# Kernel tuning notes

Measured on AMD Instinct MI355X. Metric: run time of the kernel, lower is better.

## Reference

```python
import jax, jax.numpy as jnp
import numpy as np

N = 8192  # input_size
DT = 1.0
TAU1, TAU2, TAU3 = 20.0, 50.0, 100.0


def _corr(a, b):
    # Pearson correlation of two equal-length vectors (torch.corrcoef[0,1]), NaN -> 0
    ac = a - jnp.mean(a)
    bc = b - jnp.mean(b)
    c = jnp.sum(ac * bc) / jnp.sqrt(jnp.sum(ac * ac) * jnp.sum(bc * bc))
    return jnp.where(jnp.isnan(c), jnp.zeros_like(c), c)


def setup_inputs() -> dict:
    key = jax.random.key(0)
    ks = jax.random.split(key, 8)
    return {
        'sensory_motor_input': jax.random.normal(ks[0], (N,), jnp.float32),
        'layer1_state': jax.random.normal(ks[1], (N,), jnp.float32),
        'layer2_state': jax.random.normal(ks[2], (N // 2,), jnp.float32),
        'layer3_state': jax.random.normal(ks[3], (N // 4,), jnp.float32),
        'w12': jax.random.normal(ks[4], (N // 2, N), jnp.float32) * 0.1,
        'w23': jax.random.normal(ks[5], (N // 4, N // 2), jnp.float32) * 0.1,
        'w32': jax.random.normal(ks[6], (N // 2, N // 4), jnp.float32) * 0.1,
        'w21': jax.random.normal(ks[7], (N, N // 2), jnp.float32) * 0.1,
        'correlation_strength': jnp.zeros((), jnp.float32),
        'neural_coherence': jnp.zeros((), jnp.float32),
    }


def reference(sensory_motor_input, layer1_state, layer2_state, layer3_state,
              w12, w23, w32, w21, correlation_strength, neural_coherence):
    # Layer 1: direct sensorimotor, exponential decay toward tanh target
    l1_target = jnp.tanh(sensory_motor_input)
    d1 = 1.0 - DT / TAU1
    l1 = d1 * layer1_state + (1.0 - d1) * l1_target

    # Layer 2: bottom-up + 0.3 * top-down feedback
    l2_in = w12 @ l1 + 0.3 * (w32 @ layer3_state)
    d2 = 1.0 - DT / TAU2
    l2 = d2 * layer2_state + (1.0 - d2) * jnp.tanh(l2_in)

    # Layer 3: meta feedback
    d3 = 1.0 - DT / TAU3
    l3 = d3 * layer3_state + (1.0 - d3) * jnp.tanh(w23 @ l2)

    # Cross-layer correlations (truncate the larger vector)
    c12 = _corr(l1[: l2.shape[0]], l2)
    c23 = _corr(l2[: l3.shape[0]], l3)
    corr_new = 0.9 * correlation_strength + 0.1 * (c12 + c23) / 2.0

    total_activity = jnp.sum(jnp.abs(l1)) + jnp.sum(jnp.abs(l2)) + jnp.sum(jnp.abs(l3))
    activity_variance = jnp.var(jnp.concatenate([l1, l2, l3]), ddof=1)  # torch.var unbiased
    coherence = total_activity / (activity_variance + 1e-6)
    coh_new = 0.9 * neural_coherence + 0.1 * jnp.clip(coherence, 0.0, 10.0)

    hier_activity = total_activity / (N + N // 2 + N // 4)
    return (l1, l2, l3, corr_new, coh_new, hier_activity)
```

## Files before the change

### kernel.cpp

```cpp
#include <hip/hip_runtime.h>
#include <math.h>

#define N1 8192
#define N2 4096
#define N3 2048

typedef float f4 __attribute__((ext_vector_type(4)));

__global__ __launch_bounds__(256) void k_l1(const float* __restrict__ smi,
                                            const float* __restrict__ l1s,
                                            float* __restrict__ l1) {
    int i = blockIdx.x * 256 + threadIdx.x;
    if (i < N1) l1[i] = 0.95f * l1s[i] + 0.05f * tanhf(smi[i]);
}

__global__ __launch_bounds__(256) void k_l2(const float* __restrict__ w12,
                                            const float* __restrict__ w32,
                                            const float* __restrict__ l1,
                                            const float* __restrict__ l3s,
                                            const float* __restrict__ l2s,
                                            float* __restrict__ l2) {
    __shared__ float ws[4][2];
    const int r0 = blockIdx.x * 2;
    const int t = threadIdx.x;
    const f4* __restrict__ w12r0 = reinterpret_cast<const f4*>(w12) + (size_t)r0 * (N1 / 4);
    const f4* __restrict__ w12r1 = w12r0 + (N1 / 4);
    const f4* __restrict__ w32r0 = reinterpret_cast<const f4*>(w32) + (size_t)r0 * (N3 / 4);
    const f4* __restrict__ w32r1 = w32r0 + (N3 / 4);
    const f4* __restrict__ x1 = reinterpret_cast<const f4*>(l1);
    const f4* __restrict__ x3 = reinterpret_cast<const f4*>(l3s);

    float a0 = 0.0f, a1 = 0.0f, b0 = 0.0f, b1 = 0.0f;
#pragma unroll
    for (int k = 0; k < (N1 / 4) / 256; ++k) {
        const int i = t + k * 256;
        f4 x = x1[i];
        f4 u = __builtin_nontemporal_load(&w12r0[i]);
        f4 v = __builtin_nontemporal_load(&w12r1[i]);
        a0 = fmaf(u.x, x.x, fmaf(u.y, x.y, fmaf(u.z, x.z, fmaf(u.w, x.w, a0))));
        a1 = fmaf(v.x, x.x, fmaf(v.y, x.y, fmaf(v.z, x.z, fmaf(v.w, x.w, a1))));
    }
#pragma unroll
    for (int k = 0; k < (N3 / 4) / 256; ++k) {
        const int i = t + k * 256;
        f4 x = x3[i];
        f4 u = __builtin_nontemporal_load(&w32r0[i]);
        f4 v = __builtin_nontemporal_load(&w32r1[i]);
        b0 = fmaf(u.x, x.x, fmaf(u.y, x.y, fmaf(u.z, x.z, fmaf(u.w, x.w, b0))));
        b1 = fmaf(v.x, x.x, fmaf(v.y, x.y, fmaf(v.z, x.z, fmaf(v.w, x.w, b1))));
    }
    float v0 = fmaf(0.3f, b0, a0);
    float v1 = fmaf(0.3f, b1, a1);
#pragma unroll
    for (int off = 32; off; off >>= 1) {
        v0 += __shfl_down(v0, off, 64);
        v1 += __shfl_down(v1, off, 64);
    }
    if ((t & 63) == 0) { ws[t >> 6][0] = v0; ws[t >> 6][1] = v1; }
    __syncthreads();
    if (t == 0) {
        float t0 = ws[0][0] + ws[1][0] + ws[2][0] + ws[3][0];
        float t1 = ws[0][1] + ws[1][1] + ws[2][1] + ws[3][1];
        l2[r0]     = 0.98f * l2s[r0]     + 0.02f * tanhf(t0);
        l2[r0 + 1] = 0.98f * l2s[r0 + 1] + 0.02f * tanhf(t1);
    }
}

__global__ __launch_bounds__(256) void k_l3(const float* __restrict__ w23,
                                            const float* __restrict__ l2,
                                            const float* __restrict__ l3s,
                                            float* __restrict__ l3) {
    __shared__ float ws[4][2];
    const int r0 = blockIdx.x * 2;
    const int t = threadIdx.x;
    const f4* __restrict__ wr0 = reinterpret_cast<const f4*>(w23) + (size_t)r0 * (N2 / 4);
    const f4* __restrict__ wr1 = wr0 + (N2 / 4);
    const f4* __restrict__ x2 = reinterpret_cast<const f4*>(l2);

    float a0 = 0.0f, a1 = 0.0f;
#pragma unroll
    for (int k = 0; k < (N2 / 4) / 256; ++k) {
        const int i = t + k * 256;
        f4 x = x2[i];
        f4 u = __builtin_nontemporal_load(&wr0[i]);
        f4 v = __builtin_nontemporal_load(&wr1[i]);
        a0 = fmaf(u.x, x.x, fmaf(u.y, x.y, fmaf(u.z, x.z, fmaf(u.w, x.w, a0))));
        a1 = fmaf(v.x, x.x, fmaf(v.y, x.y, fmaf(v.z, x.z, fmaf(v.w, x.w, a1))));
    }
#pragma unroll
    for (int off = 32; off; off >>= 1) {
        a0 += __shfl_down(a0, off, 64);
        a1 += __shfl_down(a1, off, 64);
    }
    if ((t & 63) == 0) { ws[t >> 6][0] = a0; ws[t >> 6][1] = a1; }
    __syncthreads();
    if (t == 0) {
        float t0 = ws[0][0] + ws[1][0] + ws[2][0] + ws[3][0];
        float t1 = ws[0][1] + ws[1][1] + ws[2][1] + ws[3][1];
        l3[r0]     = 0.99f * l3s[r0]     + 0.01f * tanhf(t0);
        l3[r0 + 1] = 0.99f * l3s[r0 + 1] + 0.01f * tanhf(t1);
    }
}

__global__ __launch_bounds__(1024) void k_fin(const float* __restrict__ out,
                                              const float* __restrict__ corr_in,
                                              const float* __restrict__ coh_in,
                                              float* __restrict__ scal) {
    __shared__ double sred[16][13];
    __shared__ double fin[13];
    const int t = threadIdx.x;
    const f4* __restrict__ o4 = reinterpret_cast<const f4*>(out);

    double p[13];
#pragma unroll
    for (int j = 0; j < 13; ++j) p[j] = 0.0;

    for (int i = t; i < 3584; i += 1024) {
        f4 v = o4[i];
#pragma unroll
        for (int c = 0; c < 4; ++c) {
            double d = (double)v[c];
            p[0] += fabs(d); p[1] += d; p[2] += d * d;
        }
    }
    {
        f4 x = o4[t];
        f4 y = o4[2048 + t];
#pragma unroll
        for (int c = 0; c < 4; ++c) {
            double dx = (double)x[c], dy = (double)y[c];
            p[3] += dx; p[4] += dy; p[5] += dx * dx; p[6] += dy * dy; p[7] += dx * dy;
        }
    }
    if (t < 512) {
        f4 x = o4[2048 + t];
        f4 y = o4[3072 + t];
#pragma unroll
        for (int c = 0; c < 4; ++c) {
            double dx = (double)x[c], dy = (double)y[c];
            p[8] += dx; p[9] += dy; p[10] += dx * dx; p[11] += dy * dy; p[12] += dx * dy;
        }
    }

#pragma unroll
    for (int j = 0; j < 13; ++j) {
        double v = p[j];
#pragma unroll
        for (int off = 32; off; off >>= 1) v += __shfl_down(v, off, 64);
        p[j] = v;
    }
    if ((t & 63) == 0) {
        const int w = t >> 6;
#pragma unroll
        for (int j = 0; j < 13; ++j) sred[w][j] = p[j];
    }
    __syncthreads();
    if (t < 13) {
        double s = 0.0;
#pragma unroll
        for (int w = 0; w < 16; ++w) s += sred[w][t];
        fin[t] = s;
    }
    __syncthreads();

    if (t == 0) {
        const double n12 = (double)N2;
        const double n23 = (double)N3;
        const double nall = (double)(N1 + N2 + N3);

        double sxy12 = fin[7] - fin[3] * fin[4] / n12;
        double sxx12 = fin[5] - fin[3] * fin[3] / n12;
        double syy12 = fin[6] - fin[4] * fin[4] / n12;
        double den12 = sqrt(sxx12 * syy12);
        double c12 = (den12 > 0.0 && isfinite(den12)) ? sxy12 / den12 : 0.0;

        double sxy23 = fin[12] - fin[8] * fin[9] / n23;
        double sxx23 = fin[10] - fin[8] * fin[8] / n23;
        double syy23 = fin[11] - fin[9] * fin[9] / n23;
        double den23 = sqrt(sxx23 * syy23);
        double c23 = (den23 > 0.0 && isfinite(den23)) ? sxy23 / den23 : 0.0;

        double corr_new = 0.9 * (double)corr_in[0] + 0.1 * (c12 + c23) * 0.5;

        double total = fin[0];
        double var = (fin[2] - fin[1] * fin[1] / nall) / (nall - 1.0);
        double coh = total / (var + 1e-6);
        coh = fmin(fmax(coh, 0.0), 10.0);
        double coh_new = 0.9 * (double)coh_in[0] + 0.1 * coh;

        scal[0] = (float)corr_new;
        scal[1] = (float)coh_new;
        scal[2] = (float)(total / nall);
    }
}

extern "C" void kernel_launch(void* const* d_in, const int* in_sizes, int n_in,
                              void* d_out, int out_size, void* d_ws, size_t ws_size,
                              hipStream_t stream) {
    const float* smi     = (const float*)d_in[0];
    const float* l1s     = (const float*)d_in[1];
    const float* l2s     = (const float*)d_in[2];
    const float* l3s     = (const float*)d_in[3];
    const float* w12     = (const float*)d_in[4];
    const float* w23     = (const float*)d_in[5];
    const float* w32     = (const float*)d_in[6];
    const float* corr_in = (const float*)d_in[8];
    const float* coh_in  = (const float*)d_in[9];

    float* out = (float*)d_out;
    float* l1 = out;
    float* l2 = out + N1;
    float* l3 = out + N1 + N2;
    float* scal = out + N1 + N2 + N3;

    k_l1<<<dim3(N1 / 256), dim3(256), 0, stream>>>(smi, l1s, l1);
    k_l2<<<dim3(N2 / 2), dim3(256), 0, stream>>>(w12, w32, l1, l3s, l2s, l2);
    k_l3<<<dim3(N3 / 2), dim3(256), 0, stream>>>(w23, l2, l3s, l3);
    k_fin<<<dim3(1), dim3(1024), 0, stream>>>(out, corr_in, coh_in, scal);
}
```

Before: 49.92 us.

## Move top-down w32 GEMV into layer-1 kernel and process four rows per block

The w32·l3 product depends only on inputs, so it is now computed in the same launch as the layer-1 update and stored in workspace. The layer-2 kernel then only streams w12 and adds the precomputed term. All GEMV kernels now handle four rows per block instead of two, which halves the grid size and reuses each input-vector load across more rows. This adds a workspace round trip, and fewer blocks could reduce memory-level parallelism.

```diff
diff --git a/kernel.cpp b/kernel.cpp
--- a/kernel.cpp
+++ b/kernel.cpp
@@ -7,62 +7,102 @@
 
 typedef float f4 __attribute__((ext_vector_type(4)));
 
-__global__ __launch_bounds__(256) void k_l1(const float* __restrict__ smi,
-                                            const float* __restrict__ l1s,
-                                            float* __restrict__ l1) {
-    int i = blockIdx.x * 256 + threadIdx.x;
-    if (i < N1) l1[i] = 0.95f * l1s[i] + 0.05f * tanhf(smi[i]);
+__global__ __launch_bounds__(256) void k_pre(const float* __restrict__ smi,
+                                             const float* __restrict__ l1s,
+                                             float* __restrict__ l1,
+                                             const float* __restrict__ w32,
+                                             const float* __restrict__ l3s,
+                                             float* __restrict__ t2) {
+    const int b = blockIdx.x;
+    const int t = threadIdx.x;
+    if (b < 32) {
+        const int i = b * 256 + t;
+        l1[i] = 0.95f * l1s[i] + 0.05f * tanhf(smi[i]);
+        return;
+    }
+    __shared__ float ws[4][4];
+    const int r0 = (b - 32) * 4;
+    const f4* __restrict__ w0 = reinterpret_cast<const f4*>(w32) + (size_t)r0 * (N3 / 4);
+    const f4* __restrict__ w1 = w0 + (N3 / 4);
+    const f4* __restrict__ w2 = w1 + (N3 / 4);
+    const f4* __restrict__ w3 = w2 + (N3 / 4);
+    const f4* __restrict__ x = reinterpret_cast<const f4*>(l3s);
+
+    float a0 = 0.f, a1 = 0.f, a2 = 0.f, a3 = 0.f;
+#pragma unroll
+    for (int k = 0; k < (N3 / 4) / 256; ++k) {
+        const int i = t + k * 256;
+        f4 xv = x[i];
+        f4 u0 = __builtin_nontemporal_load(&w0[i]);
+        f4 u1 = __builtin_nontemporal_load(&w1[i]);
+        f4 u2 = __builtin_nontemporal_load(&w2[i]);
+        f4 u3 = __builtin_nontemporal_load(&w3[i]);
+        a0 = fmaf(u0.x, xv.x, fmaf(u0.y, xv.y, fmaf(u0.z, xv.z, fmaf(u0.w, xv.w, a0))));
+        a1 = fmaf(u1.x, xv.x, fmaf(u1.y, xv.y, fmaf(u1.z, xv.z, fmaf(u1.w, xv.w, a1))));
+        a2 = fmaf(u2.x, xv.x, fmaf(u2.y, xv.y, fmaf(u2.z, xv.z, fmaf(u2.w, xv.w, a2))));
+        a3 = fmaf(u3.x, xv.x, fmaf(u3.y, xv.y, fmaf(u3.z, xv.z, fmaf(u3.w, xv.w, a3))));
+    }
+#pragma unroll
+    for (int off = 32; off; off >>= 1) {
+        a0 += __shfl_down(a0, off, 64);
+        a1 += __shfl_down(a1, off, 64);
+        a2 += __shfl_down(a2, off, 64);
+        a3 += __shfl_down(a3, off, 64);
+    }
+    if ((t & 63) == 0) {
+        const int w = t >> 6;
+        ws[w][0] = a0; ws[w][1] = a1; ws[w][2] = a2; ws[w][3] = a3;
+    }
+    __syncthreads();
+    if (t < 4) {
+        t2[r0 + t] = ws[0][t] + ws[1][t] + ws[2][t] + ws[3][t];
+    }
 }
 
 __global__ __launch_bounds__(256) void k_l2(const float* __restrict__ w12,
-                                            const float* __restrict__ w32,
                                             const float* __restrict__ l1,
-                                            const float* __restrict__ l3s,
+                                            const float* __restrict__ t2,
                                             const float* __restrict__ l2s,
                                             float* __restrict__ l2) {
-    __shared__ float ws[4][2];
-    const int r0 = blockIdx.x * 2;
-    const int t = threadIdx.x;
-    const f4* __restrict__ w12r0 = reinterpret_cast<const f4*>(w12) + (size_t)r0 * (N1 / 4);
-    const f4* __restrict__ w12r1 = w12r0 + (N1 / 4);
-    const f4* __restrict__ w32r0 = reinterpret_cast<const f4*>(w32) + (size_t)r0 * (N3 / 4);
-    const f4* __restrict__ w32r1 = w32r0 + (N3 / 4);
-    const f4* __restrict__ x1 = reinterpret_cast<const f4*>(l1);
-    const f4* __restrict__ x3 = reinterpret_cast<const f4*>(l3s);
-
-    float a0 = 0.0f, a1 = 0.0f, b0 = 0.0f, b1 = 0.0f;
+    __shared__ float ws[4][4];
+    const int r0 = blockIdx.x * 4;
+    const int t = threadIdx.x;
+    const f4* __restrict__ w0 = reinterpret_cast<const f4*>(w12) + (size_t)r0 * (N1 / 4);
+    const f4* __restrict__ w1 = w0 + (N1 / 4);
+    const f4* __restrict__ w2 = w1 + (N1 / 4);
+    const f4* __restrict__ w3 = w2 + (N1 / 4);
+    const f4* __restrict__ x = reinterpret_cast<const f4*>(l1);
+
+    float a0 = 0.f, a1 = 0.f, a2 = 0.f, a3 = 0.f;
 #pragma unroll
     for (int k = 0; k < (N1 / 4) / 256; ++k) {
         const int i = t + k * 256;
-        f4 x = x1[i];
-        f4 u = __builtin_nontemporal_load(&w12r0[i]);
-        f4 v = __builtin_nontemporal_load(&w12r1[i]);
-        a0 = fmaf(u.x, x.x, fmaf(u.y, x.y, fmaf(u.z, x.z, fmaf(u.w, x.w, a0))));
-        a1 = fmaf(v.x, x.x, fmaf(v.y, x.y, fmaf(v.z, x.z, fmaf(v.w, x.w, a1))));
-    }
-#pragma unroll
-    for (int k = 0; k < (N3 / 4) / 256; ++k) {
-        const int i = t + k * 256;
-        f4 x = x3[i];
-        f4 u = __builtin_nontemporal_load(&w32r0[i]);
-        f4 v = __builtin_nontemporal_load(&w32r1[i]);
-        b0 = fmaf(u.x, x.x, fmaf(u.y, x.y, fmaf(u.z, x.z, fmaf(u.w, x.w, b0))));
-        b1 = fmaf(v.x, x.x, fmaf(v.y, x.y, fmaf(v.z, x.z, fmaf(v.w, x.w, b1))));
-    }
-    float v0 = fmaf(0.3f, b0, a0);
-    float v1 = fmaf(0.3f, b1, a1);
+        f4 xv = x[i];
+        f4 u0 = __builtin_nontemporal_load(&w0[i]);
+        f4 u1 = __builtin_nontemporal_load(&w1[i]);
+        f4 u2 = __builtin_nontemporal_load(&w2[i]);
+        f4 u3 = __builtin_nontemporal_load(&w3[i]);
+        a0 = fmaf(u0.x, xv.x, fmaf(u0.y, xv.y, fmaf(u0.z, xv.z, fmaf(u0.w, xv.w, a0))));
+        a1 = fmaf(u1.x, xv.x, fmaf(u1.y, xv.y, fmaf(u1.z, xv.z, fmaf(u1.w, xv.w, a1))));
+        a2 = fmaf(u2.x, xv.x, fmaf(u2.y, xv.y, fmaf(u2.z, xv.z, fmaf(u2.w, xv.w, a2))));
+        a3 = fmaf(u3.x, xv.x, fmaf(u3.y, xv.y, fmaf(u3.z, xv.z, fmaf(u3.w, xv.w, a3))));
+    }
 #pragma unroll
     for (int off = 32; off; off >>= 1) {
-        v0 += __shfl_down(v0, off, 64);
-        v1 += __shfl_down(v1, off, 64);
-    }
-    if ((t & 63) == 0) { ws[t >> 6][0] = v0; ws[t >> 6][1] = v1; }
-    __syncthreads();
-    if (t == 0) {
-        float t0 = ws[0][0] + ws[1][0] + ws[2][0] + ws[3][0];
-        float t1 = ws[0][1] + ws[1][1] + ws[2][1] + ws[3][1];
-        l2[r0]     = 0.98f * l2s[r0]     + 0.02f * tanhf(t0);
-        l2[r0 + 1] = 0.98f * l2s[r0 + 1] + 0.02f * tanhf(t1);
+        a0 += __shfl_down(a0, off, 64);
+        a1 += __shfl_down(a1, off, 64);
+        a2 += __shfl_down(a2, off, 64);
+        a3 += __shfl_down(a3, off, 64);
+    }
+    if ((t & 63) == 0) {
+        const int w = t >> 6;
+        ws[w][0] = a0; ws[w][1] = a1; ws[w][2] = a2; ws[w][3] = a3;
+    }
+    __syncthreads();
+    if (t < 4) {
+        const int r = r0 + t;
+        float tot = ws[0][t] + ws[1][t] + ws[2][t] + ws[3][t] + 0.3f * t2[r];
+        l2[r] = 0.98f * l2s[r] + 0.02f * tanhf(tot);
     }
 }
 
@@ -70,35 +110,45 @@
                                             const float* __restrict__ l2,
                                             const float* __restrict__ l3s,
                                             float* __restrict__ l3) {
-    __shared__ float ws[4][2];
-    const int r0 = blockIdx.x * 2;
-    const int t = threadIdx.x;
-    const f4* __restrict__ wr0 = reinterpret_cast<const f4*>(w23) + (size_t)r0 * (N2 / 4);
-    const f4* __restrict__ wr1 = wr0 + (N2 / 4);
-    const f4* __restrict__ x2 = reinterpret_cast<const f4*>(l2);
-
-    float a0 = 0.0f, a1 = 0.0f;
+    __shared__ float ws[4][4];
+    const int r0 = blockIdx.x * 4;
+    const int t = threadIdx.x;
+    const f4* __restrict__ w0 = reinterpret_cast<const f4*>(w23) + (size_t)r0 * (N2 / 4);
+    const f4* __restrict__ w1 = w0 + (N2 / 4);
+    const f4* __restrict__ w2 = w1 + (N2 / 4);
+    const f4* __restrict__ w3 = w2 + (N2 / 4);
+    const f4* __restrict__ x = reinterpret_cast<const f4*>(l2);
+
+    float a0 = 0.f, a1 = 0.f, a2 = 0.f, a3 = 0.f;
 #pragma unroll
     for (int k = 0; k < (N2 / 4) / 256; ++k) {
         const int i = t + k * 256;
-        f4 x = x2[i];
-        f4 u = __builtin_nontemporal_load(&wr0[i]);
-        f4 v = __builtin_nontemporal_load(&wr1[i]);
-        a0 = fmaf(u.x, x.x, fmaf(u.y, x.y, fmaf(u.z, x.z, fmaf(u.w, x.w, a0))));
-        a1 = fmaf(v.x, x.x, fmaf(v.y, x.y, fmaf(v.z, x.z, fmaf(v.w, x.w, a1))));
+        f4 xv = x[i];
+        f4 u0 = __builtin_nontemporal_load(&w0[i]);
+        f4 u1 = __builtin_nontemporal_load(&w1[i]);
+        f4 u2 = __builtin_nontemporal_load(&w2[i]);
+        f4 u3 = __builtin_nontemporal_load(&w3[i]);
+        a0 = fmaf(u0.x, xv.x, fmaf(u0.y, xv.y, fmaf(u0.z, xv.z, fmaf(u0.w, xv.w, a0))));
+        a1 = fmaf(u1.x, xv.x, fmaf(u1.y, xv.y, fmaf(u1.z, xv.z, fmaf(u1.w, xv.w, a1))));
+        a2 = fmaf(u2.x, xv.x, fmaf(u2.y, xv.y, fmaf(u2.z, xv.z, fmaf(u2.w, xv.w, a2))));
+        a3 = fmaf(u3.x, xv.x, fmaf(u3.y, xv.y, fmaf(u3.z, xv.z, fmaf(u3.w, xv.w, a3))));
     }
 #pragma unroll
     for (int off = 32; off; off >>= 1) {
         a0 += __shfl_down(a0, off, 64);
         a1 += __shfl_down(a1, off, 64);
-    }
-    if ((t & 63) == 0) { ws[t >> 6][0] = a0; ws[t >> 6][1] = a1; }
-    __syncthreads();
-    if (t == 0) {
-        float t0 = ws[0][0] + ws[1][0] + ws[2][0] + ws[3][0];
-        float t1 = ws[0][1] + ws[1][1] + ws[2][1] + ws[3][1];
-        l3[r0]     = 0.99f * l3s[r0]     + 0.01f * tanhf(t0);
-        l3[r0 + 1] = 0.99f * l3s[r0 + 1] + 0.01f * tanhf(t1);
+        a2 += __shfl_down(a2, off, 64);
+        a3 += __shfl_down(a3, off, 64);
+    }
+    if ((t & 63) == 0) {
+        const int w = t >> 6;
+        ws[w][0] = a0; ws[w][1] = a1; ws[w][2] = a2; ws[w][3] = a3;
+    }
+    __syncthreads();
+    if (t < 4) {
+        const int r = r0 + t;
+        float tot = ws[0][t] + ws[1][t] + ws[2][t] + ws[3][t];
+        l3[r] = 0.99f * l3s[r] + 0.01f * tanhf(tot);
     }
 }
 
@@ -212,9 +262,10 @@
     float* l2 = out + N1;
     float* l3 = out + N1 + N2;
     float* scal = out + N1 + N2 + N3;
-
-    k_l1<<<dim3(N1 / 256), dim3(256), 0, stream>>>(smi, l1s, l1);
-    k_l2<<<dim3(N2 / 2), dim3(256), 0, stream>>>(w12, w32, l1, l3s, l2s, l2);
-    k_l3<<<dim3(N3 / 2), dim3(256), 0, stream>>>(w23, l2, l3s, l3);
+    float* t2 = (float*)d_ws;
+
+    k_pre<<<dim3(32 + N2 / 4), dim3(256), 0, stream>>>(smi, l1s, l1, w32, l3s, t2);
+    k_l2<<<dim3(N2 / 4), dim3(256), 0, stream>>>(w12, l1, t2, l2s, l2);
+    k_l3<<<dim3(N3 / 4), dim3(256), 0, stream>>>(w23, l2, l3s, l3);
     k_fin<<<dim3(1), dim3(1024), 0, stream>>>(out, corr_in, coh_in, scal);
 }
```

After: 48.43 us, median of 2. 3.0% less time.
